# Kernel tuning notes

Hardware: AMD Instinct MI355X
Metric: run time of the kernel (lower is better)

Reference implementation:

```python
import jax, jax.numpy as jnp
import numpy as np

K = 2  # DGL TAGConv default number of hops
N_GRAPHS = 64


def _tag_conv(h, src, dst, W, b, norm):
    # TAGConv: concat [h, A_hat h, A_hat^2 h] @ W + b, A_hat = D^-1/2 A D^-1/2
    n = h.shape[0]
    hops = [h]
    cur = h
    for _ in range(K):
        msg = (cur * norm)[src]                      # gather from src, [E, d]
        agg = jnp.zeros_like(cur).at[dst].add(msg)   # scatter-sum to dst
        cur = agg * norm
        hops.append(cur)
    z = jnp.concatenate(hops, axis=-1)               # [N, (K+1)*d]
    return jax.nn.relu(z @ W + b)


def _norm(dst, n):
    deg = jnp.zeros((n,), jnp.float32).at[dst].add(1.0)
    deg = jnp.clip(deg, 1.0, None)
    return (deg ** -0.5)[:, None]                    # [N, 1]


def setup_inputs() -> dict:
    key = jax.random.key(0)
    ks = jax.random.split(key, 8)
    N, E, IN, HID, C = 100000, 3200000, 128, 256, 10
    h = jax.random.normal(ks[0], (N, IN), jnp.float32)
    src = jax.random.randint(ks[1], (E,), 0, N, jnp.int32)
    dst = jax.random.randint(ks[2], (E,), 0, N, jnp.int32)
    graph_ids = jnp.sort(jax.random.randint(ks[3], (N,), 0, N_GRAPHS, jnp.int32))
    s1 = ((K + 1) * IN) ** -0.5
    s2 = ((K + 1) * HID) ** -0.5
    W1 = jax.random.normal(ks[4], ((K + 1) * IN, HID), jnp.float32) * s1
    b1 = jnp.zeros((HID,), jnp.float32)
    W2 = jax.random.normal(ks[5], ((K + 1) * HID, HID), jnp.float32) * s2
    b2 = jnp.zeros((HID,), jnp.float32)
    Wc = jax.random.normal(ks[6], (HID, C), jnp.float32) * (HID ** -0.5)
    bc = jnp.zeros((C,), jnp.float32)
    return {"h": h, "src": src, "dst": dst, "graph_ids": graph_ids,
            "W1": W1, "b1": b1, "W2": W2, "b2": b2, "Wc": Wc, "bc": bc}


def reference(h, src, dst, graph_ids, W1, b1, W2, b2, Wc, bc):
    n = h.shape[0]
    norm = _norm(dst, n)
    x = _tag_conv(h, src, dst, W1, b1, norm)
    x = _tag_conv(x, src, dst, W2, b2, norm)
    pooled = jax.ops.segment_max(x, graph_ids, num_segments=N_GRAPHS)  # [G, HID]
    return pooled @ Wc + bc                                            # [G, C]
```

## Files before the change

kernel.cpp:

```cpp
#include <hip/hip_runtime.h>
#include <hip/hip_bf16.h>


typedef unsigned short u16;
typedef unsigned int u32;

__device__ inline float u2f(u16 u) { return __uint_as_float(((u32)u) << 16); }
__device__ inline u16 f2u(float f) {
    __hip_bfloat16 b = __float2bfloat16(f);
    return *reinterpret_cast<u16*>(&b);
}


constexpr int NPB = 128, NC = 128, NBMAX = 784;

__global__ __launch_bounds__(256) void countA_kernel(
    const int* __restrict__ dst, int* __restrict__ Hmat, int E, int CS, int NB) {
    __shared__ int hist[NBMAX];
    int tid = threadIdx.x;
    for (int b = tid; b < NB; b += 256) hist[b] = 0;
    __syncthreads();
    int base = blockIdx.x * CS;
    int end = base + CS < E ? base + CS : E;
    for (int i = base + tid; i < end; i += 256) {
        int d = __builtin_nontemporal_load(dst + i);
        atomicAdd(&hist[d >> 7], 1);
    }
    __syncthreads();
    for (int b = tid; b < NB; b += 256) Hmat[b * NC + blockIdx.x] = hist[b];
}

__global__ __launch_bounds__(256) void scatterC_kernel(
    const int* __restrict__ src, const int* __restrict__ dst,
    const int* __restrict__ Omat, uint2* __restrict__ Earr,
    int E, int CS, int NB) {
    __shared__ int cur[NBMAX];
    int tid = threadIdx.x;
    int c = blockIdx.x;
    for (int b = tid; b < NB; b += 256) cur[b] = Omat[b * NC + c];
    __syncthreads();
    int base = c * CS;
    int end = base + CS < E ? base + CS : E;
    for (int i = base + tid; i < end; i += 256) {
        int d = __builtin_nontemporal_load(dst + i);
        int s = __builtin_nontemporal_load(src + i);
        int pos = atomicAdd(&cur[d >> 7], 1);
        uint2 e;
        e.x = (u32)s;
        e.y = (u32)(d & (NPB - 1));
        Earr[pos] = e;
    }
}

__global__ __launch_bounds__(256) void fineD_kernel(
    const uint2* __restrict__ Earr, const int* __restrict__ Omat,
    int* __restrict__ colidx, int* __restrict__ rowptr,
    float* __restrict__ normv, int N, int E, int NB) {
    __shared__ int cnt[NPB];
    __shared__ int scn[NPB];
    __shared__ int cur2[NPB];
    int tid = threadIdx.x;
    int b = blockIdx.x;
    int base = Omat[b * NC];
    int end = Omat[(b + 1) * NC];
    if (tid < NPB) cnt[tid] = 0;
    __syncthreads();
    for (int i = base + tid; i < end; i += 256)
        atomicAdd(&cnt[Earr[i].y], 1);
    __syncthreads();
    if (tid < NPB) scn[tid] = cnt[tid];
    __syncthreads();
    for (int off = 1; off < NPB; off <<= 1) {
        int v = (tid < NPB && tid >= off) ? scn[tid - off] : 0;
        __syncthreads();
        if (tid < NPB) scn[tid] += v;
        __syncthreads();
    }
    int node0 = b * NPB;
    if (tid < NPB) {
        int excl = scn[tid] - cnt[tid];
        cur2[tid] = base + excl;
        int node = node0 + tid;
        if (node < N) {
            rowptr[node] = base + excl;
            int d = cnt[tid];
            float fd = d < 1 ? 1.0f : (float)d;
            normv[node] = rsqrtf(fd);
        }
    }
    if (b == 0 && tid == 0) rowptr[N] = E;
    __syncthreads();
    for (int i = base + tid; i < end; i += 256) {
        uint2 e = Earr[i];
        int pos = atomicAdd(&cur2[e.y], 1);
        colidx[pos] = (int)e.x;
    }
}

__global__ void scan1_kernel(const int* __restrict__ in, int* __restrict__ outp,
                             int* __restrict__ bsum, int n) {
    __shared__ int sd[1024];
    int t = threadIdx.x;
    int i = blockIdx.x * 1024 + t;
    int v = (i < n) ? in[i] : 0;
    sd[t] = v;
    __syncthreads();
    for (int off = 1; off < 1024; off <<= 1) {
        int x = (t >= off) ? sd[t - off] : 0;
        __syncthreads();
        sd[t] += x;
        __syncthreads();
    }
    if (i < n) outp[i] = sd[t] - v;
    if (t == 1023) bsum[blockIdx.x] = sd[t];
}

__global__ void scan2_kernel(int* __restrict__ bsum, int nb) {
    __shared__ int sd[1024];
    int t = threadIdx.x;
    int v = (t < nb) ? bsum[t] : 0;
    sd[t] = v;
    __syncthreads();
    for (int off = 1; off < 1024; off <<= 1) {
        int x = (t >= off) ? sd[t - off] : 0;
        __syncthreads();
        sd[t] += x;
        __syncthreads();
    }
    if (t < nb) bsum[t] = sd[t] - v;
}

__global__ void scan3_kernel(int* __restrict__ outp, const int* __restrict__ bsum,
                             int n, int E) {
    int i = blockIdx.x * blockDim.x + threadIdx.x;
    if (i < n) outp[i] += bsum[i >> 10];
    if (i == 0) outp[n] = E;
}


struct alignas(4) U2 { u16 v[2]; };
struct alignas(8) U4 { u16 v[4]; };

__global__ void cast_kernel(const float* __restrict__ h, u16* __restrict__ cat,
                            int ngroups, int in4, int ldcat) {
    int i = blockIdx.x * blockDim.x + threadIdx.x;
    if (i < ngroups) {
        int r = i / in4, c4 = i % in4;
        float4 f = *(const float4*)(h + (size_t)i * 4);
        U4 o;
        o.v[0] = f2u(f.x); o.v[1] = f2u(f.y); o.v[2] = f2u(f.z); o.v[3] = f2u(f.w);
        *(U4*)(cat + (size_t)r * ldcat + c4 * 4) = o;
    }
}


__global__ __launch_bounds__(256) void quant_f32_128(
    const float* __restrict__ x, const float* __restrict__ normv,
    signed char* __restrict__ q, float* __restrict__ m, int N) {
    int row = blockIdx.x * 4 + (threadIdx.x >> 6);
    if (row >= N) return;
    int lane = threadIdx.x & 63;
    float2 f = *(const float2*)(x + (size_t)row * 128 + lane * 2);
    float mx = fmaxf(fabsf(f.x), fabsf(f.y));
    #pragma unroll
    for (int off = 32; off > 0; off >>= 1)
        mx = fmaxf(mx, __shfl_xor(mx, off, 64));
    float inv = mx > 0.f ? 127.f / mx : 0.f;
    char2 o;
    o.x = (signed char)(int)rintf(f.x * inv);
    o.y = (signed char)(int)rintf(f.y * inv);
    *(char2*)(q + (size_t)row * 128 + lane * 2) = o;
    if (lane == 0) m[row] = normv[row] * (mx * (1.f / 127.f));
}

__global__ __launch_bounds__(256) void quant_bf16_128(
    const u16* __restrict__ x, int ldx, const float* __restrict__ normv,
    signed char* __restrict__ q, float* __restrict__ m, int N) {
    int row = blockIdx.x * 4 + (threadIdx.x >> 6);
    if (row >= N) return;
    int lane = threadIdx.x & 63;
    U2 v = *(const U2*)(x + (size_t)row * ldx + lane * 2);
    float f0 = u2f(v.v[0]), f1 = u2f(v.v[1]);
    float mx = fmaxf(fabsf(f0), fabsf(f1));
    #pragma unroll
    for (int off = 32; off > 0; off >>= 1)
        mx = fmaxf(mx, __shfl_xor(mx, off, 64));
    float inv = mx > 0.f ? 127.f / mx : 0.f;
    char2 o;
    o.x = (signed char)(int)rintf(f0 * inv);
    o.y = (signed char)(int)rintf(f1 * inv);
    *(char2*)(q + (size_t)row * 128 + lane * 2) = o;
    if (lane == 0) m[row] = normv[row] * (mx * (1.f / 127.f));
}

__global__ __launch_bounds__(256) void quant_bf16_256(
    const u16* __restrict__ x, const float* __restrict__ normv,
    signed char* __restrict__ q, float* __restrict__ m, int N) {
    int row = blockIdx.x * 4 + (threadIdx.x >> 6);
    if (row >= N) return;
    int lane = threadIdx.x & 63;
    U4 v = *(const U4*)(x + (size_t)row * 256 + lane * 4);
    float f[4];
    #pragma unroll
    for (int i = 0; i < 4; ++i) f[i] = u2f(v.v[i]);
    float mx = fmaxf(fmaxf(fabsf(f[0]), fabsf(f[1])),
                     fmaxf(fabsf(f[2]), fabsf(f[3])));
    #pragma unroll
    for (int off = 32; off > 0; off >>= 1)
        mx = fmaxf(mx, __shfl_xor(mx, off, 64));
    float inv = mx > 0.f ? 127.f / mx : 0.f;
    char4 o;
    o.x = (signed char)(int)rintf(f[0] * inv);
    o.y = (signed char)(int)rintf(f[1] * inv);
    o.z = (signed char)(int)rintf(f[2] * inv);
    o.w = (signed char)(int)rintf(f[3] * inv);
    *(char4*)(q + (size_t)row * 256 + lane * 4) = o;
    if (lane == 0) m[row] = normv[row] * (mx * (1.f / 127.f));
}


template <int FPL>
__global__ __launch_bounds__(256) void prop_q8_kernel(
    const signed char* __restrict__ qin, const float* __restrict__ m,
    u16* __restrict__ out, int ldout,
    const int* __restrict__ rowptr, const int* __restrict__ colidx,
    const float* __restrict__ normv, int N) {
    const int D = 64 * FPL;
    int node = blockIdx.x * 4 + (threadIdx.x >> 6);
    if (node >= N) return;
    int lane = threadIdx.x & 63;
    const signed char* ip = qin + lane * FPL;
    int s = rowptr[node], e = rowptr[node + 1];
    float acc[FPL];
    #pragma unroll
    for (int q = 0; q < FPL; ++q) acc[q] = 0.f;
    int p = s;
    for (; p + 8 <= e; p += 8) {
        int c[8];
        #pragma unroll
        for (int j = 0; j < 8; ++j) c[j] = colidx[p + j];
        int w[8];
        #pragma unroll
        for (int j = 0; j < 8; ++j) {
            if (FPL == 4) w[j] = *(const int*)(ip + (size_t)c[j] * D);
            else          w[j] = *(const unsigned short*)(ip + (size_t)c[j] * D);
        }
        float nm[8];
        #pragma unroll
        for (int j = 0; j < 8; ++j) nm[j] = m[c[j]];
        #pragma unroll
        for (int j = 0; j < 8; ++j) {
            acc[0] += nm[j] * (float)(signed char)(w[j]);
            acc[1] += nm[j] * (float)(signed char)(w[j] >> 8);
            if (FPL == 4) {
                acc[2] += nm[j] * (float)(signed char)(w[j] >> 16);
                acc[3] += nm[j] * (float)(w[j] >> 24);
            }
        }
    }
    for (; p < e; ++p) {
        int c = colidx[p];
        int w;
        if (FPL == 4) w = *(const int*)(ip + (size_t)c * D);
        else          w = *(const unsigned short*)(ip + (size_t)c * D);
        float nm = m[c];
        acc[0] += nm * (float)(signed char)(w);
        acc[1] += nm * (float)(signed char)(w >> 8);
        if (FPL == 4) {
            acc[2] += nm * (float)(signed char)(w >> 16);
            acc[3] += nm * (float)(w >> 24);
        }
    }
    float nn = normv[node];
    if (FPL == 4) {
        U4 o;
        #pragma unroll
        for (int q = 0; q < 4; ++q) o.v[q] = f2u(nn * acc[q]);
        *(U4*)(out + (size_t)node * ldout + lane * 4) = o;
    } else {
        U2 o;
        o.v[0] = f2u(nn * acc[0]);
        o.v[1] = f2u(nn * acc[1]);
        *(U2*)(out + (size_t)node * ldout + lane * 2) = o;
    }
}


typedef __attribute__((ext_vector_type(8))) short bf16x8f;
typedef __attribute__((ext_vector_type(4))) float f32x4;

__device__ inline void async16(const void* g, void* l) {
    __builtin_amdgcn_global_load_lds(
        (__attribute__((address_space(1))) void*)(g),
        (__attribute__((address_space(3))) void*)(l), 16, 0, 0);
}

constexpr int GBM = 128, GBN = 64, GBK = 32;

__device__ inline void stageA_sw(const u16* __restrict__ A, int lda, int row0,
                                 int k0, u16* dst, int tid) {
    #pragma unroll
    for (int i = 0; i < 2; ++i) {
        int c = tid + i * 256;
        int row = c >> 2;
        int seg = (c & 3) ^ ((row >> 1) & 3);
        async16(A + (size_t)(row0 + row) * lda + k0 + seg * 8, dst + c * 8);
    }
}

template <int KK>
__global__ __launch_bounds__(256) void gemm_mfma(
    const u16* __restrict__ A, int lda,
    const u16* __restrict__ Bt,
    const u16* __restrict__ Cadd,
    const float* __restrict__ bias,
    u16* __restrict__ Cout,
    int M, int relu) {
    constexpr int KC = KK / 8;
    __shared__ u16 Ab[2][GBM * GBK];
    __shared__ u16 Bs[GBN * KK];
    const int tid = threadIdx.x;
    const int lane = tid & 63;
    const int wave = tid >> 6;
    const int wm = wave >> 1, wn = wave & 1;
    const int row0 = blockIdx.x * GBM;
    const int col0 = blockIdx.y * GBN;
    const int NOUT = 256;

    {
        const u16* srcB = Bt + (size_t)col0 * KK;
        #pragma unroll
        for (int i = 0; i < GBN * KC / 256; ++i) {
            int cb = tid + i * 256;
            int n = cb / KC;
            int j = (cb % KC) ^ (n & 7);
            async16(srcB + (size_t)n * KK + j * 8, &Bs[cb * 8]);
        }
    }
    stageA_sw(A, lda, row0, 0, Ab[0], tid);
    __syncthreads();

    f32x4 acc[4][2];
    #pragma unroll
    for (int mi = 0; mi < 4; ++mi)
        #pragma unroll
        for (int ni = 0; ni < 2; ++ni) acc[mi][ni] = (f32x4)0.f;

    constexpr int nk = KK / GBK;
    const int mb = lane & 15;
    const int seg = lane >> 4;
    for (int ks = 0; ks < nk; ++ks) {
        int cur = ks & 1;
        if (ks + 1 < nk) stageA_sw(A, lda, row0, (ks + 1) * GBK, Ab[cur ^ 1], tid);
        bf16x8f a[4], b[2];
        #pragma unroll
        for (int mi = 0; mi < 4; ++mi) {
            int r = wm * 64 + mi * 16 + mb;
            int ca = r * 4 + (seg ^ ((r >> 1) & 3));
            a[mi] = *(const bf16x8f*)&Ab[cur][ca * 8];
        }
        #pragma unroll
        for (int ni = 0; ni < 2; ++ni) {
            int n = wn * 32 + ni * 16 + mb;
            int jk = ks * 4 + seg;
            int cb = n * KC + (jk ^ (n & 7));
            b[ni] = *(const bf16x8f*)&Bs[cb * 8];
        }
        #pragma unroll
        for (int mi = 0; mi < 4; ++mi)
            #pragma unroll
            for (int ni = 0; ni < 2; ++ni)
                acc[mi][ni] = __builtin_amdgcn_mfma_f32_16x16x32_bf16(
                    a[mi], b[ni], acc[mi][ni], 0, 0, 0);
        __syncthreads();
    }

    #pragma unroll
    for (int mi = 0; mi < 4; ++mi) {
        #pragma unroll
        for (int r = 0; r < 4; ++r) {
            int row = row0 + wm * 64 + mi * 16 + (lane >> 4) * 4 + r;
            if (row < M) {
                #pragma unroll
                for (int ni = 0; ni < 2; ++ni) {
                    int col = col0 + wn * 32 + ni * 16 + (lane & 15);
                    float v = acc[mi][ni][r];
                    if (Cadd) v += u2f(Cadd[(size_t)row * NOUT + col]);
                    if (bias) v += bias[col];
                    if (relu) v = fmaxf(v, 0.f);
                    Cout[(size_t)row * NOUT + col] = f2u(v);
                }
            }
        }
    }
}

__global__ void transpose_cast(const float* __restrict__ W, u16* __restrict__ Wt,
                               int K, int Nn) {
    int idx = blockIdx.x * blockDim.x + threadIdx.x;
    if (idx < K * Nn) {
        int n = idx / K, k = idx % K;
        Wt[idx] = f2u(W[(size_t)k * Nn + n]);
    }
}


__global__ void pool_kernel(const u16* __restrict__ x, const int* __restrict__ gid,
                            float* __restrict__ pooled, int N, int HID) {
    int t = threadIdx.x;
    int n0 = blockIdx.x * 128;
    int n1 = n0 + 128 < N ? n0 + 128 : N;
    float cur = 0.f;
    int cg = gid[n0];
    for (int n = n0; n < n1; ++n) {
        int g = gid[n];
        if (g != cg) {
            atomicMax((int*)&pooled[(size_t)cg * HID + t], __float_as_int(cur));
            cg = g;
            cur = 0.f;
        }
        float v = u2f(x[(size_t)n * HID + t]);
        cur = cur > v ? cur : v;
    }
    atomicMax((int*)&pooled[(size_t)cg * HID + t], __float_as_int(cur));
}

__global__ void head_kernel(const float* __restrict__ pooled, const float* __restrict__ Wc,
                            const float* __restrict__ bc, float* __restrict__ out,
                            int HID, int C) {
    __shared__ float row[256];
    int g = blockIdx.x;
    int t = threadIdx.x;
    if (t < HID) row[t] = pooled[(size_t)g * HID + t];
    __syncthreads();
    if (t < C) {
        float s = bc[t];
        for (int k = 0; k < HID; ++k) s += row[k] * Wc[(size_t)k * C + t];
        out[(size_t)g * C + t] = s;
    }
}


extern "C" void kernel_launch(void* const* d_in, const int* in_sizes, int n_in,
                              void* d_out, int out_size, void* d_ws, size_t ws_size,
                              hipStream_t stream) {
    const float* h  = (const float*)d_in[0];
    const int* src  = (const int*)d_in[1];
    const int* dst  = (const int*)d_in[2];
    const int* gid  = (const int*)d_in[3];
    const float* W1 = (const float*)d_in[4];
    const float* b1 = (const float*)d_in[5];
    const float* W2 = (const float*)d_in[6];
    const float* b2 = (const float*)d_in[7];
    const float* Wc = (const float*)d_in[8];
    const float* bc = (const float*)d_in[9];
    float* out = (float*)d_out;

    const int N   = in_sizes[3];
    const int E   = in_sizes[1];
    const int IN  = in_sizes[0] / N;
    const int HID = in_sizes[5];
    const int C   = in_sizes[9];
    const int G   = out_size / C;
    const int CAT = 3 * IN;
    const int Mpad = (N + 127) & ~127;
    const int NB = (N + NPB - 1) / NPB;
    const int CS = (E + NC - 1) / NC;

    char* wp = (char*)d_ws;
    auto alloc = [&](size_t bytes) {
        char* p = wp;
        wp += (bytes + 255) & ~(size_t)255;
        return p;
    };
    float* pooled = (float*)alloc((size_t)G * HID * sizeof(float));
    float* normv  = (float*)alloc((size_t)N * sizeof(float));
    float* mv     = (float*)alloc((size_t)N * sizeof(float));
    int* rowptr   = (int*)alloc((size_t)(N + 1) * sizeof(int));
    int* bsum     = (int*)alloc(1024 * sizeof(int));
    int* Omat     = (int*)alloc((size_t)(NB * NC + 1) * sizeof(int));
    int* Hmat     = (int*)alloc((size_t)(NB * NC) * sizeof(int));
    int* colidx   = (int*)alloc((size_t)E * sizeof(int));
    u16* Wt1      = (u16*)alloc((size_t)CAT * HID * sizeof(u16));
    u16* Wt2      = (u16*)alloc((size_t)3 * HID * HID * sizeof(u16));
    u16* CAT1     = (u16*)alloc((size_t)Mpad * CAT * sizeof(u16));
    u16* X1       = (u16*)alloc((size_t)Mpad * HID * sizeof(u16));
    u16* B2       = (u16*)alloc((size_t)Mpad * HID * sizeof(u16));
    u16* B1       = CAT1;
    uint2* Earr   = (uint2*)CAT1;
    signed char* Q8L2 = (signed char*)(CAT1 + (size_t)Mpad * HID);
    signed char* Q8L1 = (signed char*)B2;

    const int n2 = NB * NC;
    countA_kernel<<<NC, 256, 0, stream>>>(dst, Hmat, E, CS, NB);
    scan1_kernel<<<(n2 + 1023) / 1024, 1024, 0, stream>>>(Hmat, Omat, bsum, n2);
    scan2_kernel<<<1, 1024, 0, stream>>>(bsum, (n2 + 1023) / 1024);
    scan3_kernel<<<(n2 + 255) / 256, 256, 0, stream>>>(Omat, bsum, n2, E);
    scatterC_kernel<<<NC, 256, 0, stream>>>(src, dst, Omat, Earr, E, CS, NB);
    fineD_kernel<<<NB, 256, 0, stream>>>(Earr, Omat, colidx, rowptr, normv, N, E, NB);

    transpose_cast<<<(CAT * HID + 255) / 256, 256, 0, stream>>>(W1, Wt1, CAT, HID);
    for (int s2 = 0; s2 < 3; ++s2)
        transpose_cast<<<(HID * HID + 255) / 256, 256, 0, stream>>>(
            W2 + (size_t)s2 * HID * HID, Wt2 + (size_t)s2 * HID * HID, HID, HID);

    {
        int ngroups = N * (IN / 4);
        cast_kernel<<<(ngroups + 255) / 256, 256, 0, stream>>>(h, CAT1, ngroups, IN / 4, CAT);
    }
    int pb = (N + 3) / 4;
    quant_f32_128<<<pb, 256, 0, stream>>>(h, normv, Q8L1, mv, N);
    prop_q8_kernel<2><<<pb, 256, 0, stream>>>(Q8L1, mv, CAT1 + IN, CAT,
                                              rowptr, colidx, normv, N);
    quant_bf16_128<<<pb, 256, 0, stream>>>(CAT1 + IN, CAT, normv, Q8L1, mv, N);
    prop_q8_kernel<2><<<pb, 256, 0, stream>>>(Q8L1, mv, CAT1 + 2 * IN, CAT,
                                              rowptr, colidx, normv, N);
    dim3 ggrid(Mpad / GBM, HID / GBN);
    gemm_mfma<384><<<ggrid, 256, 0, stream>>>(CAT1, CAT, Wt1, nullptr, b1, X1, N, 1);

    gemm_mfma<256><<<ggrid, 256, 0, stream>>>(X1, HID, Wt2 + (size_t)2 * HID * HID,
                                              nullptr, nullptr, B1, N, 0);
    quant_bf16_256<<<pb, 256, 0, stream>>>(B1, normv, Q8L2, mv, N);
    prop_q8_kernel<4><<<pb, 256, 0, stream>>>(Q8L2, mv, B2, HID,
                                              rowptr, colidx, normv, N);
    gemm_mfma<256><<<ggrid, 256, 0, stream>>>(X1, HID, Wt2 + (size_t)HID * HID,
                                              B2, nullptr, B1, N, 0);
    quant_bf16_256<<<pb, 256, 0, stream>>>(B1, normv, Q8L2, mv, N);
    prop_q8_kernel<4><<<pb, 256, 0, stream>>>(Q8L2, mv, B2, HID,
                                              rowptr, colidx, normv, N);
    gemm_mfma<256><<<ggrid, 256, 0, stream>>>(X1, HID, Wt2, B2, b2, B1, N, 1);

    hipMemsetAsync(pooled, 0, (size_t)G * HID * sizeof(float), stream);
    pool_kernel<<<(N + 127) / 128, HID, 0, stream>>>(B1, gid, pooled, N, HID);
    head_kernel<<<G, HID, 0, stream>>>(pooled, Wc, bc, out, HID, C);
}
```

Baseline: 1.166 ms.

## Split wavefront across two edges per step, fuse cast/quant and hop-quantization into propagation

Propagation now has each half-wavefront handle alternate edges with wider per-lane loads (4 or 8 bytes), then combines the halves with a cross-lane shuffle. Quantization switches to offset-unsigned bytes, with the offset removed through a running sum of scales. The fp32-to-bf16 cast is merged into the first quantization, and the first layer's second-hop quantization is produced directly inside the first propagation, dropping two kernels and one bf16 re-read. The intent is fewer, larger gather transactions and less intermediate traffic. The costs are more registers and a shuffle reduction per node.

```diff
diff --git a/kernel.cpp b/kernel.cpp
--- a/kernel.cpp
+++ b/kernel.cpp
@@ -4,6 +4,7 @@
 
 typedef unsigned short u16;
 typedef unsigned int u32;
+typedef unsigned char u8;
 
 __device__ inline float u2f(u16 u) { return __uint_as_float(((u32)u) << 16); }
 __device__ inline u16 f2u(float f) {
@@ -140,62 +141,37 @@
 
 struct alignas(4) U2 { u16 v[2]; };
 struct alignas(8) U4 { u16 v[4]; };
-
-__global__ void cast_kernel(const float* __restrict__ h, u16* __restrict__ cat,
-                            int ngroups, int in4, int ldcat) {
-    int i = blockIdx.x * blockDim.x + threadIdx.x;
-    if (i < ngroups) {
-        int r = i / in4, c4 = i % in4;
-        float4 f = *(const float4*)(h + (size_t)i * 4);
-        U4 o;
-        o.v[0] = f2u(f.x); o.v[1] = f2u(f.y); o.v[2] = f2u(f.z); o.v[3] = f2u(f.w);
-        *(U4*)(cat + (size_t)r * ldcat + c4 * 4) = o;
-    }
-}
-
-
-__global__ __launch_bounds__(256) void quant_f32_128(
-    const float* __restrict__ x, const float* __restrict__ normv,
-    signed char* __restrict__ q, float* __restrict__ m, int N) {
+struct alignas(16) U8 { u16 v[8]; };
+
+
+__global__ __launch_bounds__(256) void castquant_f32_128(
+    const float* __restrict__ h, u16* __restrict__ cat, int ldcat,
+    const float* __restrict__ normv,
+    u8* __restrict__ q, float* __restrict__ m, int N) {
     int row = blockIdx.x * 4 + (threadIdx.x >> 6);
     if (row >= N) return;
     int lane = threadIdx.x & 63;
-    float2 f = *(const float2*)(x + (size_t)row * 128 + lane * 2);
+    float2 f = *(const float2*)(h + (size_t)row * 128 + lane * 2);
+    U2 o;
+    o.v[0] = f2u(f.x);
+    o.v[1] = f2u(f.y);
+    *(U2*)(cat + (size_t)row * ldcat + lane * 2) = o;
     float mx = fmaxf(fabsf(f.x), fabsf(f.y));
     #pragma unroll
     for (int off = 32; off > 0; off >>= 1)
         mx = fmaxf(mx, __shfl_xor(mx, off, 64));
     float inv = mx > 0.f ? 127.f / mx : 0.f;
-    char2 o;
-    o.x = (signed char)(int)rintf(f.x * inv);
-    o.y = (signed char)(int)rintf(f.y * inv);
-    *(char2*)(q + (size_t)row * 128 + lane * 2) = o;
+    u32 q0 = (u32)((int)rintf(f.x * inv) + 128);
+    u32 q1 = (u32)((int)rintf(f.y * inv) + 128);
+    *(unsigned short*)(q + (size_t)row * 128 + lane * 2) =
+        (unsigned short)(q0 | (q1 << 8));
     if (lane == 0) m[row] = normv[row] * (mx * (1.f / 127.f));
 }
 
-__global__ __launch_bounds__(256) void quant_bf16_128(
-    const u16* __restrict__ x, int ldx, const float* __restrict__ normv,
-    signed char* __restrict__ q, float* __restrict__ m, int N) {
-    int row = blockIdx.x * 4 + (threadIdx.x >> 6);
-    if (row >= N) return;
-    int lane = threadIdx.x & 63;
-    U2 v = *(const U2*)(x + (size_t)row * ldx + lane * 2);
-    float f0 = u2f(v.v[0]), f1 = u2f(v.v[1]);
-    float mx = fmaxf(fabsf(f0), fabsf(f1));
-    #pragma unroll
-    for (int off = 32; off > 0; off >>= 1)
-        mx = fmaxf(mx, __shfl_xor(mx, off, 64));
-    float inv = mx > 0.f ? 127.f / mx : 0.f;
-    char2 o;
-    o.x = (signed char)(int)rintf(f0 * inv);
-    o.y = (signed char)(int)rintf(f1 * inv);
-    *(char2*)(q + (size_t)row * 128 + lane * 2) = o;
-    if (lane == 0) m[row] = normv[row] * (mx * (1.f / 127.f));
-}
 
 __global__ __launch_bounds__(256) void quant_bf16_256(
     const u16* __restrict__ x, const float* __restrict__ normv,
-    signed char* __restrict__ q, float* __restrict__ m, int N) {
+    u8* __restrict__ q, float* __restrict__ m, int N) {
     int row = blockIdx.x * 4 + (threadIdx.x >> 6);
     if (row >= N) return;
     int lane = threadIdx.x & 63;
@@ -209,79 +185,134 @@
     for (int off = 32; off > 0; off >>= 1)
         mx = fmaxf(mx, __shfl_xor(mx, off, 64));
     float inv = mx > 0.f ? 127.f / mx : 0.f;
-    char4 o;
-    o.x = (signed char)(int)rintf(f[0] * inv);
-    o.y = (signed char)(int)rintf(f[1] * inv);
-    o.z = (signed char)(int)rintf(f[2] * inv);
-    o.w = (signed char)(int)rintf(f[3] * inv);
-    *(char4*)(q + (size_t)row * 256 + lane * 4) = o;
+    u32 b0 = (u32)((int)rintf(f[0] * inv) + 128);
+    u32 b1 = (u32)((int)rintf(f[1] * inv) + 128);
+    u32 b2 = (u32)((int)rintf(f[2] * inv) + 128);
+    u32 b3 = (u32)((int)rintf(f[3] * inv) + 128);
+    *(u32*)(q + (size_t)row * 256 + lane * 4) =
+        b0 | (b1 << 8) | (b2 << 16) | (b3 << 24);
     if (lane == 0) m[row] = normv[row] * (mx * (1.f / 127.f));
 }
 
 
-template <int FPL>
+template <int BPL, int QOUT>
 __global__ __launch_bounds__(256) void prop_q8_kernel(
-    const signed char* __restrict__ qin, const float* __restrict__ m,
+    const u8* __restrict__ qin, const float* __restrict__ m,
     u16* __restrict__ out, int ldout,
     const int* __restrict__ rowptr, const int* __restrict__ colidx,
-    const float* __restrict__ normv, int N) {
-    const int D = 64 * FPL;
+    const float* __restrict__ normv, int N,
+    u8* __restrict__ qout, float* __restrict__ mout) {
+    constexpr int D = 32 * BPL;
+    constexpr int NW = BPL / 4;
     int node = blockIdx.x * 4 + (threadIdx.x >> 6);
     if (node >= N) return;
-    int lane = threadIdx.x & 63;
-    const signed char* ip = qin + lane * FPL;
+    const int lane = threadIdx.x & 63;
+    const int half = lane >> 5;
+    const int l32 = lane & 31;
+    const u32 laneoff = (u32)l32 * BPL;
     int s = rowptr[node], e = rowptr[node + 1];
-    float acc[FPL];
-    #pragma unroll
-    for (int q = 0; q < FPL; ++q) acc[q] = 0.f;
+    float acc[BPL];
+    #pragma unroll
+    for (int q = 0; q < BPL; ++q) acc[q] = 0.f;
+    float msum = 0.f;
     int p = s;
     for (; p + 8 <= e; p += 8) {
-        int c[8];
-        #pragma unroll
-        for (int j = 0; j < 8; ++j) c[j] = colidx[p + j];
-        int w[8];
-        #pragma unroll
-        for (int j = 0; j < 8; ++j) {
-            if (FPL == 4) w[j] = *(const int*)(ip + (size_t)c[j] * D);
-            else          w[j] = *(const unsigned short*)(ip + (size_t)c[j] * D);
-        }
-        float nm[8];
-        #pragma unroll
-        for (int j = 0; j < 8; ++j) nm[j] = m[c[j]];
-        #pragma unroll
-        for (int j = 0; j < 8; ++j) {
-            acc[0] += nm[j] * (float)(signed char)(w[j]);
-            acc[1] += nm[j] * (float)(signed char)(w[j] >> 8);
-            if (FPL == 4) {
-                acc[2] += nm[j] * (float)(signed char)(w[j] >> 16);
-                acc[3] += nm[j] * (float)(w[j] >> 24);
+        int c[4];
+        #pragma unroll
+        for (int u = 0; u < 4; ++u) c[u] = colidx[p + 2 * u + half];
+        u32 w[4][NW];
+        #pragma unroll
+        for (int u = 0; u < 4; ++u) {
+            u32 off = (u32)c[u] * D + laneoff;
+            if (BPL == 8) {
+                uint2 g = *(const uint2*)(qin + off);
+                w[u][0] = g.x; w[u][1] = g.y;
+            } else {
+                w[u][0] = *(const u32*)(qin + off);
             }
         }
-    }
-    for (; p < e; ++p) {
-        int c = colidx[p];
-        int w;
-        if (FPL == 4) w = *(const int*)(ip + (size_t)c * D);
-        else          w = *(const unsigned short*)(ip + (size_t)c * D);
-        float nm = m[c];
-        acc[0] += nm * (float)(signed char)(w);
-        acc[1] += nm * (float)(signed char)(w >> 8);
-        if (FPL == 4) {
-            acc[2] += nm * (float)(signed char)(w >> 16);
-            acc[3] += nm * (float)(w >> 24);
-        }
-    }
+        float nm[4];
+        #pragma unroll
+        for (int u = 0; u < 4; ++u) nm[u] = m[c[u]];
+        #pragma unroll
+        for (int u = 0; u < 4; ++u) {
+            msum += nm[u];
+            #pragma unroll
+            for (int t = 0; t < NW; ++t) {
+                u32 ww = w[u][t];
+                acc[4 * t + 0] += nm[u] * (float)(ww & 0xffu);
+                acc[4 * t + 1] += nm[u] * (float)((ww >> 8) & 0xffu);
+                acc[4 * t + 2] += nm[u] * (float)((ww >> 16) & 0xffu);
+                acc[4 * t + 3] += nm[u] * (float)(ww >> 24);
+            }
+        }
+    }
+    for (; p < e; p += 2) {
+        int idx = p + half;
+        int v = idx < e;
+        int c = colidx[v ? idx : e - 1];
+        float nm = v ? m[c] : 0.f;
+        u32 off = (u32)c * D + laneoff;
+        u32 w[NW];
+        if (BPL == 8) {
+            uint2 g = *(const uint2*)(qin + off);
+            w[0] = g.x; w[1] = g.y;
+        } else {
+            w[0] = *(const u32*)(qin + off);
+        }
+        msum += nm;
+        #pragma unroll
+        for (int t = 0; t < NW; ++t) {
+            u32 ww = w[t];
+            acc[4 * t + 0] += nm * (float)(ww & 0xffu);
+            acc[4 * t + 1] += nm * (float)((ww >> 8) & 0xffu);
+            acc[4 * t + 2] += nm * (float)((ww >> 16) & 0xffu);
+            acc[4 * t + 3] += nm * (float)(ww >> 24);
+        }
+    }
+    #pragma unroll
+    for (int q = 0; q < BPL; ++q) acc[q] += __shfl_xor(acc[q], 32, 64);
+    msum += __shfl_xor(msum, 32, 64);
     float nn = normv[node];
-    if (FPL == 4) {
-        U4 o;
-        #pragma unroll
-        for (int q = 0; q < 4; ++q) o.v[q] = f2u(nn * acc[q]);
-        *(U4*)(out + (size_t)node * ldout + lane * 4) = o;
-    } else {
-        U2 o;
-        o.v[0] = f2u(nn * acc[0]);
-        o.v[1] = f2u(nn * acc[1]);
-        *(U2*)(out + (size_t)node * ldout + lane * 2) = o;
+    #pragma unroll
+    for (int q = 0; q < BPL; ++q) acc[q] = nn * (acc[q] - 128.f * msum);
+    if (half == 0) {
+        if (BPL == 8) {
+            U8 o;
+            #pragma unroll
+            for (int q = 0; q < 8; ++q) o.v[q] = f2u(acc[q]);
+            *(U8*)(out + (size_t)node * ldout + l32 * 8) = o;
+        } else {
+            U4 o;
+            #pragma unroll
+            for (int q = 0; q < 4; ++q) o.v[q] = f2u(acc[q]);
+            *(U4*)(out + (size_t)node * ldout + l32 * 4) = o;
+        }
+    }
+    if (QOUT) {
+        float mx = 0.f;
+        #pragma unroll
+        for (int q = 0; q < BPL; ++q) mx = fmaxf(mx, fabsf(acc[q]));
+        #pragma unroll
+        for (int off = 16; off > 0; off >>= 1)
+            mx = fmaxf(mx, __shfl_xor(mx, off, 64));
+        float inv = mx > 0.f ? 127.f / mx : 0.f;
+        if (half == 0) {
+            u32 b[BPL > 4 ? 8 : 4];
+            #pragma unroll
+            for (int q = 0; q < BPL; ++q)
+                b[q] = (u32)((int)rintf(acc[q] * inv) + 128);
+            if (BPL == 8) {
+                uint2 g;
+                g.x = b[0] | (b[1] << 8) | (b[2] << 16) | (b[3] << 24);
+                g.y = b[4] | (b[5] << 8) | (b[6] << 16) | (b[7] << 24);
+                *(uint2*)(qout + (size_t)node * D + l32 * 8) = g;
+            } else {
+                *(u32*)(qout + (size_t)node * D + l32 * 4) =
+                    b[0] | (b[1] << 8) | (b[2] << 16) | (b[3] << 24);
+            }
+            if (lane == 0) mout[node] = nn * (mx * (1.f / 127.f));
+        }
     }
 }
 
@@ -476,6 +507,7 @@
     float* pooled = (float*)alloc((size_t)G * HID * sizeof(float));
     float* normv  = (float*)alloc((size_t)N * sizeof(float));
     float* mv     = (float*)alloc((size_t)N * sizeof(float));
+    float* mv2    = (float*)alloc((size_t)N * sizeof(float));
     int* rowptr   = (int*)alloc((size_t)(N + 1) * sizeof(int));
     int* bsum     = (int*)alloc(1024 * sizeof(int));
     int* Omat     = (int*)alloc((size_t)(NB * NC + 1) * sizeof(int));
@@ -488,8 +520,9 @@
     u16* B2       = (u16*)alloc((size_t)Mpad * HID * sizeof(u16));
     u16* B1       = CAT1;
     uint2* Earr   = (uint2*)CAT1;
-    signed char* Q8L2 = (signed char*)(CAT1 + (size_t)Mpad * HID);
-    signed char* Q8L1 = (signed char*)B2;
+    u8* Q8L2      = (u8*)(CAT1 + (size_t)Mpad * HID);
+    u8* Q8A       = (u8*)B2;
+    u8* Q8B       = (u8*)B2 + (size_t)Mpad * 128;
 
     const int n2 = NB * NC;
     countA_kernel<<<NC, 256, 0, stream>>>(dst, Hmat, E, CS, NB);
@@ -504,30 +537,28 @@
         transpose_cast<<<(HID * HID + 255) / 256, 256, 0, stream>>>(
             W2 + (size_t)s2 * HID * HID, Wt2 + (size_t)s2 * HID * HID, HID, HID);
 
-    {
-        int ngroups = N * (IN / 4);
-        cast_kernel<<<(ngroups + 255) / 256, 256, 0, stream>>>(h, CAT1, ngroups, IN / 4, CAT);
-    }
     int pb = (N + 3) / 4;
-    quant_f32_128<<<pb, 256, 0, stream>>>(h, normv, Q8L1, mv, N);
-    prop_q8_kernel<2><<<pb, 256, 0, stream>>>(Q8L1, mv, CAT1 + IN, CAT,
-                                              rowptr, colidx, normv, N);
-    quant_bf16_128<<<pb, 256, 0, stream>>>(CAT1 + IN, CAT, normv, Q8L1, mv, N);
-    prop_q8_kernel<2><<<pb, 256, 0, stream>>>(Q8L1, mv, CAT1 + 2 * IN, CAT,
-                                              rowptr, colidx, normv, N);
+    castquant_f32_128<<<pb, 256, 0, stream>>>(h, CAT1, CAT, normv, Q8A, mv, N);
+    prop_q8_kernel<4, 1><<<pb, 256, 0, stream>>>(Q8A, mv, CAT1 + IN, CAT,
+                                                 rowptr, colidx, normv, N, Q8B, mv2);
+    prop_q8_kernel<4, 0><<<pb, 256, 0, stream>>>(Q8B, mv2, CAT1 + 2 * IN, CAT,
+                                                 rowptr, colidx, normv, N,
+                                                 nullptr, nullptr);
     dim3 ggrid(Mpad / GBM, HID / GBN);
     gemm_mfma<384><<<ggrid, 256, 0, stream>>>(CAT1, CAT, Wt1, nullptr, b1, X1, N, 1);
 
     gemm_mfma<256><<<ggrid, 256, 0, stream>>>(X1, HID, Wt2 + (size_t)2 * HID * HID,
                                               nullptr, nullptr, B1, N, 0);
     quant_bf16_256<<<pb, 256, 0, stream>>>(B1, normv, Q8L2, mv, N);
-    prop_q8_kernel<4><<<pb, 256, 0, stream>>>(Q8L2, mv, B2, HID,
-                                              rowptr, colidx, normv, N);
+    prop_q8_kernel<8, 0><<<pb, 256, 0, stream>>>(Q8L2, mv, B2, HID,
+                                                 rowptr, colidx, normv, N,
+                                                 nullptr, nullptr);
     gemm_mfma<256><<<ggrid, 256, 0, stream>>>(X1, HID, Wt2 + (size_t)HID * HID,
                                               B2, nullptr, B1, N, 0);
     quant_bf16_256<<<pb, 256, 0, stream>>>(B1, normv, Q8L2, mv, N);
-    prop_q8_kernel<4><<<pb, 256, 0, stream>>>(Q8L2, mv, B2, HID,
-                                              rowptr, colidx, normv, N);
+    prop_q8_kernel<8, 0><<<pb, 256, 0, stream>>>(Q8L2, mv, B2, HID,
+                                                 rowptr, colidx, normv, N,
+                                                 nullptr, nullptr);
     gemm_mfma<256><<<ggrid, 256, 0, stream>>>(X1, HID, Wt2, B2, b2, B1, N, 1);
 
     hipMemsetAsync(pooled, 0, (size_t)G * HID * sizeof(float), stream);
```

Result: faster. 1.102 ms (-5.4%).
